# Kernel optimization log

Measured on AMD Instinct MI355X. Metric: run time of the kernel, lower is better.

Reference implementation:

```python
import jax, jax.numpy as jnp
import numpy as np

C = 32        # latent_channels
BCH = 6       # bottleneck_channels
H, W = 180, 320
N = H * W
B = 32


def _hilbert_walk(h, w):
    """Faithful port of FlattenDeflatten._hilbert_curve: Morton/Z-order bit
    interleave over (i, j), stable-sorted by key (ties broken by raster index).
    Returns flat raster indices in walk order."""
    i = np.arange(h, dtype=np.int64)[:, None]
    j = np.arange(w, dtype=np.int64)[None, :]
    z = np.zeros((h, w), dtype=np.int64)
    for bit in range(16):
        z |= ((i >> bit) & 1) << (2 * bit + 1)
        z |= ((j >> bit) & 1) << (2 * bit)
    # coords.sort() on (z, flat_idx) == stable argsort of z over raster order
    return np.argsort(z.ravel(), kind='stable')


def setup_inputs() -> dict:
    key = jax.random.key(0)
    ks = jax.random.split(key, 6)
    walk = _hilbert_walk(H, W)
    unwalk = np.zeros_like(walk)
    unwalk[walk] = np.arange(N)
    # torch Conv1d default init: U(-1/sqrt(fan_in), 1/sqrt(fan_in)), kernel=1
    bf = 1.0 / np.sqrt(C)
    bd = 1.0 / np.sqrt(BCH)
    return {
        "latent": jax.random.normal(ks[0], (B, C, H, W), dtype=jnp.float32),
        "w_flat": jax.random.uniform(ks[1], (BCH, C), jnp.float32, -bf, bf),
        "b_flat": jax.random.uniform(ks[2], (BCH,), jnp.float32, -bf, bf),
        "w_deflat": jax.random.uniform(ks[3], (C, BCH), jnp.float32, -bd, bd),
        "b_deflat": jax.random.uniform(ks[4], (C,), jnp.float32, -bd, bd),
        "spatial_embed": jax.random.normal(ks[5], (1, C, N), dtype=jnp.float32) * 0.02,
        "walk_idx": jnp.asarray(walk, dtype=jnp.int32),
        "unwalk_idx": jnp.asarray(unwalk, dtype=jnp.int32),
    }


def reference(latent, w_flat, b_flat, w_deflat, b_deflat, spatial_embed,
              walk_idx, unwalk_idx):
    Bb, Cc, Hh, Ww = latent.shape
    # flatten: serialize along walk order, then 1x1 conv (channel GEMM)
    seq = latent.reshape(Bb, Cc, Hh * Ww)[:, :, walk_idx]          # (B, C, N)
    flat = jnp.einsum('oc,bcn->bon', w_flat, seq) + b_flat[:, None]  # (B, BCH, N)
    # deflatten: 1x1 conv back, add positional embed, inverse permutation
    dseq = (jnp.einsum('co,bon->bcn', w_deflat, flat)
            + b_deflat[:, None] + spatial_embed)                    # (B, C, N)
    recon = dseq[:, :, unwalk_idx].reshape(Bb, Cc, Hh, Ww)
    return (recon, flat)
```

## Files before the change

### kernel.cpp

```cpp
#include <hip/hip_runtime.h>

#define CCH 32
#define BCH 6
#define HH  180
#define WW  320
#define NN  (HH*WW)
#define BATCH 32
#define RPC 4
#define CHUNKS (HH/RPC)
#define THREADS 320

typedef float f32x2 __attribute__((ext_vector_type(2)));
typedef float f32x4 __attribute__((ext_vector_type(4)));

__global__ __launch_bounds__(256) void permute_se(
    const float* __restrict__ se, const int* __restrict__ unwalk,
    float* __restrict__ se_r)
{
    const int p = blockIdx.x * 256 + threadIdx.x;
    const int n = unwalk[p];
    #pragma unroll 8
    for (int c = 0; c < CCH; ++c)
        se_r[(size_t)c * NN + p] = se[(size_t)c * NN + n];
}

template<int SE_RASTER>
__global__ __launch_bounds__(THREADS) void fused_flatten_deflatten(
    const float* __restrict__ latent,
    const float* __restrict__ w_flat,
    const float* __restrict__ b_flat,
    const float* __restrict__ w_deflat,
    const float* __restrict__ b_deflat,
    const float* __restrict__ se,
    const int*   __restrict__ unwalk,
    float* __restrict__ recon,
    float* __restrict__ flat_out)
{
    __shared__ float s_wf[BCH*CCH];
    __shared__ float s_wd[CCH*BCH];
    __shared__ float s_bf[BCH];
    __shared__ float s_bd[CCH];

    const int t  = threadIdx.x;
    const int bx = blockIdx.x;
    const int r  = bx >> 5;
    const int b  = bx & 31;

    if (t < BCH*CCH) { s_wf[t] = w_flat[t]; s_wd[t] = w_deflat[t]; }
    if (t < BCH)     s_bf[t] = b_flat[t];
    if (t < CCH)     s_bd[t] = b_deflat[t];
    __syncthreads();

    const int i  = RPC*r + t/80;
    const int j  = 4*(t%80);
    const int p  = i*WW + j;

    const int nb = unwalk[(i & ~1)*WW + j];
    const int n2 = nb + 2*(i & 1);

    const float* latb   = latent + (size_t)b * (CCH*NN) + p;
    float*       reconb = recon  + (size_t)b * (CCH*NN) + p;

    float acc[BCH][4];
    #pragma unroll
    for (int o = 0; o < BCH; ++o) {
        const float bo = s_bf[o];
        acc[o][0] = bo; acc[o][1] = bo; acc[o][2] = bo; acc[o][3] = bo;
    }

    #pragma unroll 8
    for (int c = 0; c < CCH; ++c) {
        const f32x4 x = __builtin_nontemporal_load(
            reinterpret_cast<const f32x4*>(latb + (size_t)c*NN));
        #pragma unroll
        for (int o = 0; o < BCH; ++o) {
            const float w = s_wf[o*CCH + c];
            acc[o][0] += w*x.x; acc[o][1] += w*x.y;
            acc[o][2] += w*x.z; acc[o][3] += w*x.w;
        }
    }

    float* fb = flat_out + (size_t)b * (BCH*NN) + n2;
    #pragma unroll
    for (int o = 0; o < BCH; ++o) {
        f32x2 lo; lo.x = acc[o][0]; lo.y = acc[o][1];
        f32x2 hi; hi.x = acc[o][2]; hi.y = acc[o][3];
        *reinterpret_cast<f32x2*>(fb + (size_t)o*NN)     = lo;
        *reinterpret_cast<f32x2*>(fb + (size_t)o*NN + 4) = hi;
    }

    #pragma unroll 8
    for (int c = 0; c < CCH; ++c) {
        float s0, s1, s2, s3;
        if (SE_RASTER) {
            const f32x4 s4 = *reinterpret_cast<const f32x4*>(se + (size_t)c*NN + p);
            s0 = s4.x; s1 = s4.y; s2 = s4.z; s3 = s4.w;
        } else {
            const f32x2 a = *reinterpret_cast<const f32x2*>(se + (size_t)c*NN + n2);
            const f32x2 bq = *reinterpret_cast<const f32x2*>(se + (size_t)c*NN + n2 + 4);
            s0 = a.x; s1 = a.y; s2 = bq.x; s3 = bq.y;
        }
        const float bd = s_bd[c];
        float y0 = bd + s0, y1 = bd + s1, y2 = bd + s2, y3 = bd + s3;
        #pragma unroll
        for (int o = 0; o < BCH; ++o) {
            const float w = s_wd[c*BCH + o];
            y0 += w*acc[o][0]; y1 += w*acc[o][1];
            y2 += w*acc[o][2]; y3 += w*acc[o][3];
        }
        f32x4 yv; yv.x = y0; yv.y = y1; yv.z = y2; yv.w = y3;
        *reinterpret_cast<f32x4*>(reconb + (size_t)c*NN) = yv;
    }
}

extern "C" void kernel_launch(void* const* d_in, const int* in_sizes, int n_in,
                              void* d_out, int out_size, void* d_ws, size_t ws_size,
                              hipStream_t stream) {
    const float* latent   = (const float*)d_in[0];
    const float* w_flat   = (const float*)d_in[1];
    const float* b_flat   = (const float*)d_in[2];
    const float* w_deflat = (const float*)d_in[3];
    const float* b_deflat = (const float*)d_in[4];
    const float* se       = (const float*)d_in[5];
    const int*   unwalk   = (const int*)d_in[7];

    float* recon = (float*)d_out;
    float* flat  = (float*)d_out + (size_t)BATCH * CCH * NN;

    const size_t se_bytes = (size_t)CCH * NN * sizeof(float);
    dim3 grid(CHUNKS * BATCH);
    dim3 block(THREADS);

    if (ws_size >= se_bytes) {
        float* se_r = (float*)d_ws;
        permute_se<<<dim3(NN/256), dim3(256), 0, stream>>>(se, unwalk, se_r);
        fused_flatten_deflatten<1><<<grid, block, 0, stream>>>(
            latent, w_flat, b_flat, w_deflat, b_deflat, se_r, unwalk, recon, flat);
    } else {
        fused_flatten_deflatten<0><<<grid, block, 0, stream>>>(
            latent, w_flat, b_flat, w_deflat, b_deflat, se, unwalk, recon, flat);
    }
}
```

Baseline: 131.7 us.

## Stage permuted spatial embed in LDS per row, shared across batches; drop pre-permute kernel

Removes the separate kernel that permuted the spatial embedding into a workspace buffer. Each block now handles one image row for four batch items, gathers that row's embedding (with the deflatten bias folded in) into shared memory once, and reuses it across the four batches. Loops are fully unrolled and recon stores become nontemporal. This saves a kernel launch and the workspace write and read traffic, at the cost of a block-wide barrier and extra LDS per block.

```diff
diff --git a/kernel.cpp b/kernel.cpp
--- a/kernel.cpp
+++ b/kernel.cpp
@@ -6,25 +6,14 @@
 #define WW  320
 #define NN  (HH*WW)
 #define BATCH 32
-#define RPC 4
-#define CHUNKS (HH/RPC)
-#define THREADS 320
+#define NGROUPS 8
+#define GPB 4
+#define SLOTS 80
+#define THREADS (SLOTS*GPB)
 
 typedef float f32x2 __attribute__((ext_vector_type(2)));
 typedef float f32x4 __attribute__((ext_vector_type(4)));
 
-__global__ __launch_bounds__(256) void permute_se(
-    const float* __restrict__ se, const int* __restrict__ unwalk,
-    float* __restrict__ se_r)
-{
-    const int p = blockIdx.x * 256 + threadIdx.x;
-    const int n = unwalk[p];
-    #pragma unroll 8
-    for (int c = 0; c < CCH; ++c)
-        se_r[(size_t)c * NN + p] = se[(size_t)c * NN + n];
-}
-
-template<int SE_RASTER>
 __global__ __launch_bounds__(THREADS) void fused_flatten_deflatten(
     const float* __restrict__ latent,
     const float* __restrict__ w_flat,
@@ -36,28 +25,39 @@
     float* __restrict__ recon,
     float* __restrict__ flat_out)
 {
+    __shared__ float s_se[CCH*WW];
     __shared__ float s_wf[BCH*CCH];
     __shared__ float s_wd[CCH*BCH];
     __shared__ float s_bf[BCH];
-    __shared__ float s_bd[CCH];
 
-    const int t  = threadIdx.x;
-    const int bx = blockIdx.x;
-    const int r  = bx >> 5;
-    const int b  = bx & 31;
+    const int t   = threadIdx.x;
+    const int bx  = blockIdx.x;
+    const int i   = bx / NGROUPS;
+    const int grp = bx % NGROUPS;
 
     if (t < BCH*CCH) { s_wf[t] = w_flat[t]; s_wd[t] = w_deflat[t]; }
     if (t < BCH)     s_bf[t] = b_flat[t];
-    if (t < CCH)     s_bd[t] = b_deflat[t];
-    __syncthreads();
 
-    const int i  = RPC*r + t/80;
-    const int j  = 4*(t%80);
+    const int sl = t % SLOTS;
+    const int bg = t / SLOTS;
+    const int j  = 4*sl;
     const int p  = i*WW + j;
 
     const int nb = unwalk[(i & ~1)*WW + j];
     const int n2 = nb + 2*(i & 1);
 
+    #pragma unroll
+    for (int k = 0; k < 8; ++k) {
+        const int c = bg + 4*k;
+        const f32x2 a = *reinterpret_cast<const f32x2*>(se + (size_t)c*NN + n2);
+        const f32x2 d = *reinterpret_cast<const f32x2*>(se + (size_t)c*NN + n2 + 4);
+        const float bd = b_deflat[c];
+        f32x4 v; v.x = a.x + bd; v.y = a.y + bd; v.z = d.x + bd; v.w = d.y + bd;
+        *reinterpret_cast<f32x4*>(&s_se[c*WW + j]) = v;
+    }
+    __syncthreads();
+
+    const int b = grp*GPB + bg;
     const float* latb   = latent + (size_t)b * (CCH*NN) + p;
     float*       reconb = recon  + (size_t)b * (CCH*NN) + p;
 
@@ -68,7 +68,7 @@
         acc[o][0] = bo; acc[o][1] = bo; acc[o][2] = bo; acc[o][3] = bo;
     }
 
-    #pragma unroll 8
+    #pragma unroll
     for (int c = 0; c < CCH; ++c) {
         const f32x4 x = __builtin_nontemporal_load(
             reinterpret_cast<const f32x4*>(latb + (size_t)c*NN));
@@ -89,19 +89,10 @@
         *reinterpret_cast<f32x2*>(fb + (size_t)o*NN + 4) = hi;
     }
 
-    #pragma unroll 8
+    #pragma unroll
     for (int c = 0; c < CCH; ++c) {
-        float s0, s1, s2, s3;
-        if (SE_RASTER) {
-            const f32x4 s4 = *reinterpret_cast<const f32x4*>(se + (size_t)c*NN + p);
-            s0 = s4.x; s1 = s4.y; s2 = s4.z; s3 = s4.w;
-        } else {
-            const f32x2 a = *reinterpret_cast<const f32x2*>(se + (size_t)c*NN + n2);
-            const f32x2 bq = *reinterpret_cast<const f32x2*>(se + (size_t)c*NN + n2 + 4);
-            s0 = a.x; s1 = a.y; s2 = bq.x; s3 = bq.y;
-        }
-        const float bd = s_bd[c];
-        float y0 = bd + s0, y1 = bd + s1, y2 = bd + s2, y3 = bd + s3;
+        const f32x4 s4 = *reinterpret_cast<const f32x4*>(&s_se[c*WW + j]);
+        float y0 = s4.x, y1 = s4.y, y2 = s4.z, y3 = s4.w;
         #pragma unroll
         for (int o = 0; o < BCH; ++o) {
             const float w = s_wd[c*BCH + o];
@@ -109,7 +100,8 @@
             y2 += w*acc[o][2]; y3 += w*acc[o][3];
         }
         f32x4 yv; yv.x = y0; yv.y = y1; yv.z = y2; yv.w = y3;
-        *reinterpret_cast<f32x4*>(reconb + (size_t)c*NN) = yv;
+        __builtin_nontemporal_store(yv,
+            reinterpret_cast<f32x4*>(reconb + (size_t)c*NN));
     }
 }
 
@@ -127,17 +119,8 @@
     float* recon = (float*)d_out;
     float* flat  = (float*)d_out + (size_t)BATCH * CCH * NN;
 
-    const size_t se_bytes = (size_t)CCH * NN * sizeof(float);
-    dim3 grid(CHUNKS * BATCH);
+    dim3 grid(HH * NGROUPS);
     dim3 block(THREADS);
-
-    if (ws_size >= se_bytes) {
-        float* se_r = (float*)d_ws;
-        permute_se<<<dim3(NN/256), dim3(256), 0, stream>>>(se, unwalk, se_r);
-        fused_flatten_deflatten<1><<<grid, block, 0, stream>>>(
-            latent, w_flat, b_flat, w_deflat, b_deflat, se_r, unwalk, recon, flat);
-    } else {
-        fused_flatten_deflatten<0><<<grid, block, 0, stream>>>(
-            latent, w_flat, b_flat, w_deflat, b_deflat, se, unwalk, recon, flat);
-    }
+    fused_flatten_deflatten<<<grid, block, 0, stream>>>(
+        latent, w_flat, b_flat, w_deflat, b_deflat, se, unwalk, recon, flat);
 }
```

Result: faster. 118.1 us (-10.3%).
